# Performance work log

Hardware: AMD Instinct MI355X
Metric: run time of the kernel (lower is better)

The kernel has to match this reference:

```python
import jax, jax.numpy as jnp
import numpy as np

N_EMBD = 1024
N_HEAD = 16
STRIDE = 128
C = 8
SEQ = 2048
BATCH = 2


def _sparse_causal_mask(nd, ns, stride, c, dtype):
    # Faithful vectorization of _sparse_attention_mask:
    # column j is globally visible if (j % stride) >= stride - c (the last c
    # columns of each stride block), each query also sees its own stride block,
    # and everything is causally masked (j <= q).
    j = jnp.arange(ns)
    q = jnp.arange(ns)[:, None]
    col_sel = (j % stride) >= (stride - c)          # strided summary columns
    same_block = (j[None, :] // stride) == (q // stride)  # local block
    causal = j[None, :] <= q
    mask = ((col_sel[None, :] | same_block) & causal).astype(dtype)
    return mask[ns - nd:]


def setup_inputs() -> dict:
    key = jax.random.key(0)
    k1, k2, k3 = jax.random.split(key, 3)
    inputs = jax.random.normal(k1, (BATCH, SEQ, N_EMBD), dtype=jnp.float32)
    w_attn = jax.random.normal(k2, (N_EMBD, 3 * N_EMBD), dtype=jnp.float32) * 0.02
    b_attn = jnp.zeros((3 * N_EMBD,), dtype=jnp.float32)
    proj_std = 0.02 / np.sqrt(2 * 24)  # n_layer = 24
    w_proj = jax.random.normal(k3, (N_EMBD, N_EMBD), dtype=jnp.float32) * proj_std
    b_proj = jnp.zeros((N_EMBD,), dtype=jnp.float32)
    return {"inputs": inputs, "w_attn": w_attn, "b_attn": b_attn,
            "w_proj": w_proj, "b_proj": b_proj}


def reference(inputs, w_attn, b_attn, w_proj, b_proj):
    B, S, E = inputs.shape
    H = N_HEAD
    D = E // H
    qkv = inputs @ w_attn + b_attn                     # [B,S,3E]
    q, k, v = jnp.split(qkv, 3, axis=-1)
    def split_heads(x):
        return x.reshape(B, S, H, D).transpose(0, 2, 1, 3)  # [B,H,S,D]
    q, k, v = split_heads(q), split_heads(k), split_heads(v)
    present = jnp.stack([k, v], axis=1)                # [B,2,H,S,D]
    scale = jnp.asarray(D, q.dtype) ** 0.5
    w = jnp.einsum('bhqd,bhkd->bhqk', q, k) / scale    # [B,H,S,S]
    mask = _sparse_causal_mask(S, S, STRIDE, C, w.dtype)
    w = w * mask - 1e10 * (1.0 - mask)
    p = jax.nn.softmax(w, axis=-1).astype(v.dtype)
    h = jnp.einsum('bhqk,bhkd->bhqd', p, v)            # [B,H,S,D]
    h = h.transpose(0, 2, 1, 3).reshape(B, S, E)       # merge heads
    h = h @ w_proj + b_proj
    # dropout p=0.0 (eval) -> identity
    return (h, present)
```

## Files before the change

kernel.cpp:

```cpp
#include <hip/hip_runtime.h>
#include <stdint.h>

typedef unsigned short u16;
typedef unsigned int u32;
typedef __attribute__((ext_vector_type(4))) float f32x4;
typedef __attribute__((ext_vector_type(4))) u16 u16x4;
typedef __attribute__((ext_vector_type(8))) __bf16 bf16x8;

__device__ __forceinline__ u16 f2bf(float f) {
  u32 u = __builtin_bit_cast(u32, f);
  u = (u + 0x7FFFu + ((u >> 16) & 1u)) >> 16;
  return (u16)u;
}

__device__ __forceinline__ void gload_lds16(const void* g, void* l) {
  __builtin_amdgcn_global_load_lds(
      (const __attribute__((address_space(1))) void*)(uintptr_t)(g),
      (__attribute__((address_space(3))) void*)(u32)(uintptr_t)(l),
      16, 0, 0);
}

__global__ __launch_bounds__(256) void k_prep(
    const float* __restrict__ x, u16* __restrict__ xbf,
    const float* __restrict__ wa, u16* __restrict__ wat,
    const float* __restrict__ wp, u16* __restrict__ wpt) {
  __shared__ float tile[32][33];
  const int bid = blockIdx.x, t = threadIdx.x;
  if (bid < 4096) {
    int i = bid * 256 + t;
    f32x4 v = ((const f32x4*)x)[i];
    u16x4 o = { f2bf(v.x), f2bf(v.y), f2bf(v.z), f2bf(v.w) };
    ((u16x4*)xbf)[i] = o;
    return;
  }
  const float* in;
  u16* out;
  int n0, k0, N;
  if (bid < 4096 + 3072) {
    int idx = bid - 4096;
    in = wa; out = wat; N = 3072;
    n0 = (idx % 96) * 32; k0 = (idx / 96) * 32;
  } else {
    int idx = bid - 7168;
    in = wp; out = wpt; N = 1024;
    n0 = (idx & 31) * 32; k0 = (idx >> 5) * 32;
  }
  int c = t & 31, r0 = t >> 5;
#pragma unroll
  for (int i = 0; i < 4; ++i)
    tile[r0 + i * 8][c] = in[(size_t)(k0 + r0 + i * 8) * N + n0 + c];
  __syncthreads();
  int on = t >> 3, ok = (t & 7) * 4;
  u16x4 o = { f2bf(tile[ok + 0][on]), f2bf(tile[ok + 1][on]),
              f2bf(tile[ok + 2][on]), f2bf(tile[ok + 3][on]) };
  *(u16x4*)&out[(size_t)(n0 + on) * 1024 + k0 + ok] = o;
}

__global__ __launch_bounds__(256) void k_kv(const float* __restrict__ present,
                                            u16* __restrict__ kbf,
                                            u16* __restrict__ vtw) {
  __shared__ float tile[32][33];
  const int bid = blockIdx.x, t = threadIdx.x;
  if (bid >= 4096) {
    int i = bid - 4096;
    size_t idx = (size_t)i * 256 + t;
    size_t b = idx >> 19, off = idx & ((1u << 19) - 1);
    f32x4 v = ((const f32x4*)present)[b * (1u << 20) + off];
    u16x4 o = { f2bf(v.x), f2bf(v.y), f2bf(v.z), f2bf(v.w) };
    ((u16x4*)kbf)[idx] = o;
    return;
  }
  int bh = bid >> 7, rem = bid & 127;
  int s0 = (rem >> 1) * 32, d0 = (rem & 1) * 32;
  int b = bh >> 4, h = bh & 15;
  const float* vsrc = present + (((size_t)(b * 2 + 1) * 16 + h) * 2048) * 64;
  u16* vdst = vtw + ((size_t)bh * 64) * 2048;
  int c = t & 31, r0 = t >> 5;
#pragma unroll
  for (int i = 0; i < 4; ++i)
    tile[r0 + i * 8][c] = vsrc[(size_t)(s0 + r0 + i * 8) * 64 + d0 + c];
  __syncthreads();
  int on = t >> 3, ok = (t & 7) * 4;
  u16x4 o = { f2bf(tile[ok + 0][on]), f2bf(tile[ok + 1][on]),
              f2bf(tile[ok + 2][on]), f2bf(tile[ok + 3][on]) };
  *(u16x4*)&vdst[(size_t)(d0 + on) * 2048 + s0 + ok] = o;
}

__global__ __launch_bounds__(512, 1) void k_gemm256(
    const u16* __restrict__ A, const u16* __restrict__ Bt,
    const float* __restrict__ bias, u16* __restrict__ outq,
    float* __restrict__ outp) {
  __shared__ u16 a_lds[2][256 * 64];
  __shared__ u16 b_lds[2][192 * 64];
  const int t = threadIdx.x;
  const int lane = t & 63, w = t >> 6;
  const int cc = lane & 15, g = lane >> 4;
  const int wr = w >> 1, wc = w & 1;

  int f = blockIdx.y * 16 + blockIdx.x;
  int xcd = f & 7, idx = f >> 3;
  const int m0 = ((xcd >> 1) * 4 + (idx >> 3)) * 256;
  const int n0 = ((xcd & 1) * 8 + (idx & 7)) * 192;

  const int srow = t >> 3;
  const int scolb = (t & 7) * 16;
  const size_t pitch = 2048;

  auto stage = [&](int bi, int kt) {
#pragma unroll
    for (int i = 0; i < 3; ++i) {
      int row = i * 64 + srow;
      gload_lds16((const char*)Bt + (size_t)(n0 + row) * pitch + kt * 128 +
                      (scolb ^ ((row & 7) << 4)),
                  (char*)b_lds[bi] + row * 128 + scolb);
    }
#pragma unroll
    for (int i = 0; i < 4; ++i) {
      int row = i * 64 + srow;
      gload_lds16((const char*)A + (size_t)(m0 + row) * pitch + kt * 128 +
                      (scolb ^ ((row & 7) << 4)),
                  (char*)a_lds[bi] + row * 128 + scolb);
    }
  };

  auto readA = [&](bf16x8 (&af)[4], int bi, int kk) {
#pragma unroll
    for (int mf = 0; mf < 4; ++mf) {
      int row = wr * 64 + mf * 16 + cc;
      af[mf] = *(const bf16x8*)((const char*)a_lds[bi] + row * 128 +
                                ((kk * 64 + g * 16) ^ ((row & 7) << 4)));
    }
  };
  auto readB = [&](bf16x8 (&bf)[6], int bi, int kk) {
#pragma unroll
    for (int nf = 0; nf < 6; ++nf) {
      int row = wc * 96 + nf * 16 + cc;
      bf[nf] = *(const bf16x8*)((const char*)b_lds[bi] + row * 128 +
                                ((kk * 64 + g * 16) ^ ((row & 7) << 4)));
    }
  };

  f32x4 acc[4][6] = {};
  bf16x8 a0[4], b0[6], a1[4], b1[6];

  stage(0, 0);
  asm volatile("s_waitcnt vmcnt(0)\n\ts_barrier" ::: "memory");
  readA(a0, 0, 0);
  readB(b0, 0, 0);

  for (int j = 0; j < 16; ++j) {
    const int bi = j & 1, nx = bi ^ 1;
    if (j < 15) stage(nx, j + 1);
    readA(a1, bi, 1);
    readB(b1, bi, 1);

    __builtin_amdgcn_s_setprio(1);
#pragma unroll
    for (int mf = 0; mf < 4; ++mf)
#pragma unroll
      for (int nf = 0; nf < 6; ++nf)
        acc[mf][nf] = __builtin_amdgcn_mfma_f32_16x16x32_bf16(
            a0[mf], b0[nf], acc[mf][nf], 0, 0, 0);
    __builtin_amdgcn_s_setprio(0);

    __builtin_amdgcn_s_setprio(1);
#pragma unroll
    for (int mf = 0; mf < 4; ++mf)
#pragma unroll
      for (int nf = 0; nf < 6; ++nf)
        acc[mf][nf] = __builtin_amdgcn_mfma_f32_16x16x32_bf16(
            a1[mf], b1[nf], acc[mf][nf], 0, 0, 0);
    __builtin_amdgcn_s_setprio(0);

    if (j < 15) {
      asm volatile("s_waitcnt vmcnt(0) lgkmcnt(0)\n\ts_barrier" ::: "memory");
      readA(a0, nx, 0);
      readB(b0, nx, 0);
    }
  }

  float bv[6];
#pragma unroll
  for (int nf = 0; nf < 6; ++nf) bv[nf] = bias[n0 + wc * 96 + nf * 16 + cc];

#pragma unroll
  for (int mf = 0; mf < 4; ++mf)
#pragma unroll
    for (int nf = 0; nf < 6; ++nf) {
      int n = n0 + wc * 96 + nf * 16 + cc;
      int mb = m0 + wr * 64 + mf * 16 + g * 4;
      float v[4];
#pragma unroll
      for (int j = 0; j < 4; ++j) v[j] = acc[mf][nf][j] + bv[nf];
      if (n < 1024) {
#pragma unroll
        for (int j = 0; j < 4; ++j) outq[(size_t)(mb + j) * 1024 + n] = f2bf(v[j]);
      } else {
        int n2 = n - 1024;
        int kv = n2 >> 10; n2 &= 1023;
        int hh = n2 >> 6, d = n2 & 63;
        int bb = mb >> 11, ss = mb & 2047;
        float* pr = outp + ((((size_t)bb * 2 + kv) * 16 + hh) * 2048 + ss) * 64 + d;
#pragma unroll
        for (int j = 0; j < 4; ++j) pr[(size_t)j * 64] = v[j];
      }
    }
}

template <int EPI, int BN>
__global__ __launch_bounds__(256) void k_gemm(
    const u16* __restrict__ A, const u16* __restrict__ Bt,
    const float* __restrict__ bias, u16* __restrict__ outq,
    float* __restrict__ outp, int M, int N, int K) {
  __shared__ u16 a_lds[128 * 64];
  __shared__ u16 b_lds[BN * 64];
  const int t = threadIdx.x;
  const int lane = t & 63, w = t >> 6;

  int m0, n0;
  {
    constexpr int NXT = (EPI == 0) ? 24 : 16;
    constexpr int NCH = (EPI == 0) ? 12 : 8;
    int f = blockIdx.y * NXT + blockIdx.x;
    int xcd = f & 7, idx = f >> 3;
    int mt = (xcd >> 1) * 8 + idx / NCH;
    int nt = (xcd & 1) * NCH + idx % NCH;
    m0 = mt * 128;
    n0 = nt * BN;
  }

  const int srow = t >> 3;
  const int scb = (t & 7) * 16;
  const int ssw = scb ^ ((srow & 7) << 4);
  const size_t pitch = (size_t)K * 2;
  const char* aS = (const char*)A + (size_t)(m0 + srow) * pitch + ssw;
  const char* bS = (const char*)Bt + (size_t)(n0 + srow) * pitch + ssw;
  char* al = (char*)a_lds + t * 16;
  char* bl = (char*)b_lds + t * 16;
  const int wm = (w >> 1) * 64, wn = (w & 1) * (BN / 2);
  const int cc = lane & 15, g = lane >> 4;
  constexpr int NF = BN / 32;

  f32x4 acc[4][NF] = {};

  for (int kt = 0; kt < K; kt += 64) {
    __syncthreads();
#pragma unroll
    for (int i = 0; i < 4; ++i)
      gload_lds16(aS + (size_t)kt * 2 + (size_t)i * 32 * pitch, al + i * 4096);
#pragma unroll
    for (int i = 0; i < BN / 32; ++i)
      gload_lds16(bS + (size_t)kt * 2 + (size_t)i * 32 * pitch, bl + i * 4096);
    __syncthreads();
#pragma unroll
    for (int kk = 0; kk < 2; ++kk) {
      bf16x8 af[4], bf_[NF];
#pragma unroll
      for (int mf = 0; mf < 4; ++mf) {
        int row = wm + mf * 16 + cc;
        af[mf] = *(const bf16x8*)((const char*)a_lds + row * 128 +
                                  ((kk * 64 + g * 16) ^ ((row & 7) << 4)));
      }
#pragma unroll
      for (int nf = 0; nf < NF; ++nf) {
        int row = wn + nf * 16 + cc;
        bf_[nf] = *(const bf16x8*)((const char*)b_lds + row * 128 +
                                   ((kk * 64 + g * 16) ^ ((row & 7) << 4)));
      }
#pragma unroll
      for (int mf = 0; mf < 4; ++mf)
#pragma unroll
        for (int nf = 0; nf < NF; ++nf)
          acc[mf][nf] = __builtin_amdgcn_mfma_f32_16x16x32_bf16(
              af[mf], bf_[nf], acc[mf][nf], 0, 0, 0);
    }
  }

  float bv[NF];
#pragma unroll
  for (int nf = 0; nf < NF; ++nf) bv[nf] = bias[n0 + wn + nf * 16 + cc];

#pragma unroll
  for (int mf = 0; mf < 4; ++mf)
#pragma unroll
    for (int nf = 0; nf < NF; ++nf) {
      int n = n0 + wn + nf * 16 + cc;
      int mb = m0 + wm + mf * 16 + g * 4;
      float v[4];
#pragma unroll
      for (int j = 0; j < 4; ++j) v[j] = acc[mf][nf][j] + bv[nf];
      if (EPI == 1) {
#pragma unroll
        for (int j = 0; j < 4; ++j) outp[(size_t)(mb + j) * N + n] = v[j];
      } else if (n < 1024) {
#pragma unroll
        for (int j = 0; j < 4; ++j) outq[(size_t)(mb + j) * 1024 + n] = f2bf(v[j]);
      } else {
        int n2 = n - 1024;
        int kv = n2 >> 10; n2 &= 1023;
        int hh = n2 >> 6, d = n2 & 63;
        int bb = mb >> 11, ss = mb & 2047;
        float* pr = outp + ((((size_t)bb * 2 + kv) * 16 + hh) * 2048 + ss) * 64 + d;
#pragma unroll
        for (int j = 0; j < 4; ++j) pr[(size_t)j * 64] = v[j];
      }
    }
}

__global__ __launch_bounds__(256) void k_attn(
    const u16* __restrict__ qws, const u16* __restrict__ kbf,
    const u16* __restrict__ vtw, u16* __restrict__ hws) {
  const int qb = blockIdx.x, h = blockIdx.y, b = blockIdx.z;
  const int t = threadIdx.x, lane = t & 63, w = t >> 6;
  const int cc = lane & 15, g = lane >> 4;

  __shared__ u16 k_lds[256 * 64];
  __shared__ u16 p_lds[4][32 * 72];
  __shared__ float rsum[4][32];

  const char* kh = (const char*)kbf + (size_t)(b * 16 + h) * (2048 * 128);
  const char* vh = (const char*)vtw + (size_t)(b * 16 + h) * (64 * 4096);

  {
    int rr = t >> 3, seg = (t & 7) * 16;
#pragma unroll
    for (int i = 0; i < 8; ++i) {
      int r = i * 32 + rr;
      int i2 = r - 128;
      int gr = (r < 128) ? (qb * 128 + r) : ((i2 >> 3) * 128 + 120 + (i2 & 7));
      gload_lds16(kh + (size_t)gr * 128 + (seg ^ ((r & 7) << 4)),
                  (char*)k_lds + i * 4096 + t * 16);
    }
  }

  bf16x8 qf_[2][2];
  {
    const char* qsrc = (const char*)qws +
        (size_t)(b * 2048 + qb * 128 + w * 32 + cc) * 2048 + h * 128 + g * 16;
#pragma unroll
    for (int qf = 0; qf < 2; ++qf)
#pragma unroll
      for (int kk = 0; kk < 2; ++kk)
        qf_[qf][kk] = *(const bf16x8*)(qsrc + (size_t)qf * 16 * 2048 + kk * 64);
  }
  __syncthreads();

  const int nsum = 8 * qb;
  f32x4 o_[2][4] = {};
  float lsum[2] = { 0.f, 0.f };

#pragma unroll 2
  for (int ch = 0; ch < 4; ++ch) {
    f32x4 s[4][2] = {};
#pragma unroll
    for (int kf2 = 0; kf2 < 4; ++kf2) {
      int row = ch * 64 + kf2 * 16 + cc;
      const char* kr = (const char*)k_lds + row * 128;
#pragma unroll
      for (int kk = 0; kk < 2; ++kk) {
        bf16x8 kfr = *(const bf16x8*)(kr + ((kk * 64 + g * 16) ^ ((cc & 7) << 4)));
#pragma unroll
        for (int qf = 0; qf < 2; ++qf)
          s[kf2][qf] = __builtin_amdgcn_mfma_f32_16x16x32_bf16(
              kfr, qf_[qf][kk], s[kf2][qf], 0, 0, 0);
      }
    }
#pragma unroll
    for (int qf = 0; qf < 2; ++qf) {
      int q_local = w * 32 + qf * 16 + cc;
#pragma unroll
      for (int kf2 = 0; kf2 < 4; ++kf2) {
#pragma unroll
        for (int j = 0; j < 4; ++j) {
          int key = ch * 64 + kf2 * 16 + g * 4 + j;
          bool vis = (key < 128) ? (key <= q_local) : (key - 128 < nsum);
          float p = vis ? exp2f(s[kf2][qf][j] * 0.180336884f) : 0.f;
          s[kf2][qf][j] = p;
          lsum[qf] += p;
        }
        u16x4 pw = { f2bf(s[kf2][qf][0]), f2bf(s[kf2][qf][1]),
                     f2bf(s[kf2][qf][2]), f2bf(s[kf2][qf][3]) };
        *(u16x4*)&p_lds[w][(qf * 16 + cc) * 72 + kf2 * 16 + g * 4] = pw;
      }
    }
#pragma unroll
    for (int kk = 0; kk < 2; ++kk) {
      bf16x8 pa[2], vb[4];
#pragma unroll
      for (int mf = 0; mf < 2; ++mf)
        pa[mf] = *(const bf16x8*)((const char*)p_lds[w] +
                                  (mf * 16 + cc) * 144 + kk * 64 + g * 16);
      int cb = (ch < 2) ? (qb * 256 + ch * 128 + kk * 64 + g * 16)
                        : (((ch - 2) * 8 + kk * 4 + g) * 256 + 240);
#pragma unroll
      for (int nf = 0; nf < 4; ++nf)
        vb[nf] = *(const bf16x8*)(vh + (size_t)(nf * 16 + cc) * 4096 + cb);
#pragma unroll
      for (int mf = 0; mf < 2; ++mf)
#pragma unroll
        for (int nf = 0; nf < 4; ++nf)
          o_[mf][nf] = __builtin_amdgcn_mfma_f32_16x16x32_bf16(pa[mf], vb[nf],
                                                               o_[mf][nf], 0, 0, 0);
    }
  }

#pragma unroll
  for (int qf = 0; qf < 2; ++qf) {
    float sum = lsum[qf];
    sum += __shfl_xor(sum, 16);
    sum += __shfl_xor(sum, 32);
    if (g == 0) rsum[w][qf * 16 + cc] = sum;
  }
#pragma unroll
  for (int mf = 0; mf < 2; ++mf)
#pragma unroll
    for (int j = 0; j < 4; ++j) {
      float inv = 1.0f / rsum[w][mf * 16 + g * 4 + j];
      size_t row = (size_t)(b * 2048 + qb * 128 + w * 32 + mf * 16 + g * 4 + j);
#pragma unroll
      for (int nf = 0; nf < 4; ++nf)
        hws[row * 1024 + h * 64 + nf * 16 + cc] = f2bf(o_[mf][nf][j] * inv);
    }
}

extern "C" void kernel_launch(void* const* d_in, const int* in_sizes, int n_in,
                              void* d_out, int out_size, void* d_ws, size_t ws_size,
                              hipStream_t stream) {
  const float* x      = (const float*)d_in[0];
  const float* w_attn = (const float*)d_in[1];
  const float* b_attn = (const float*)d_in[2];
  const float* w_proj = (const float*)d_in[3];
  const float* b_proj = (const float*)d_in[4];
  float* h_out   = (float*)d_out;
  float* present = (float*)d_out + 4194304;

  char* ws = (char*)d_ws;
  u16* xbf = (u16*)(ws);
  u16* qws = (u16*)(ws + (8u << 20));
  u16* wat = (u16*)(ws + (16u << 20));
  u16* wpt = (u16*)(ws + (22u << 20));
  u16* kbf = (u16*)(ws + (24u << 20));
  u16* vtw = (u16*)(ws + (32u << 20));
  u16* hws = xbf;

  k_prep<<<8192, 256, 0, stream>>>(x, xbf, w_attn, wat, w_proj, wpt);
  k_gemm256<<<dim3(16, 16), 512, 0, stream>>>(xbf, wat, b_attn, qws, present);
  k_kv<<<8192, 256, 0, stream>>>(present, kbf, vtw);
  k_attn<<<dim3(16, 16, 2), 256, 0, stream>>>(qws, kbf, vtw, hws);
  k_gemm<1, 64><<<dim3(16, 32), 256, 0, stream>>>(hws, wpt, b_proj, nullptr,
                                                  h_out, 4096, 1024, 1024);
}
```

Before: 86.50 us.

## Replace double-buffered GEMM K-loop with single-buffered 128-wide K tiles

```diff
diff --git a/kernel.cpp b/kernel.cpp
--- a/kernel.cpp
+++ b/kernel.cpp
@@ -90,8 +90,8 @@
     const u16* __restrict__ A, const u16* __restrict__ Bt,
     const float* __restrict__ bias, u16* __restrict__ outq,
     float* __restrict__ outp) {
-  __shared__ u16 a_lds[2][256 * 64];
-  __shared__ u16 b_lds[2][192 * 64];
+  __shared__ u16 a_lds[256 * 128];
+  __shared__ u16 b_lds[192 * 128];
   const int t = threadIdx.x;
   const int lane = t & 63, w = t >> 6;
   const int cc = lane & 15, g = lane >> 4;
@@ -102,80 +102,54 @@
   const int m0 = ((xcd >> 1) * 4 + (idx >> 3)) * 256;
   const int n0 = ((xcd & 1) * 8 + (idx & 7)) * 192;
 
-  const int srow = t >> 3;
-  const int scolb = (t & 7) * 16;
+  const int srow = t >> 4;
+  const int scolb = (t & 15) * 16;
   const size_t pitch = 2048;
 
-  auto stage = [&](int bi, int kt) {
-#pragma unroll
-    for (int i = 0; i < 3; ++i) {
-      int row = i * 64 + srow;
-      gload_lds16((const char*)Bt + (size_t)(n0 + row) * pitch + kt * 128 +
+  auto stage = [&](int kt) {
+#pragma unroll
+    for (int i = 0; i < 8; ++i) {
+      int row = i * 32 + srow;
+      gload_lds16((const char*)A + (size_t)(m0 + row) * pitch + kt * 256 +
                       (scolb ^ ((row & 7) << 4)),
-                  (char*)b_lds[bi] + row * 128 + scolb);
-    }
-#pragma unroll
-    for (int i = 0; i < 4; ++i) {
-      int row = i * 64 + srow;
-      gload_lds16((const char*)A + (size_t)(m0 + row) * pitch + kt * 128 +
+                  (char*)a_lds + row * 256 + scolb);
+    }
+#pragma unroll
+    for (int i = 0; i < 6; ++i) {
+      int row = i * 32 + srow;
+      gload_lds16((const char*)Bt + (size_t)(n0 + row) * pitch + kt * 256 +
                       (scolb ^ ((row & 7) << 4)),
-                  (char*)a_lds[bi] + row * 128 + scolb);
+                  (char*)b_lds + row * 256 + scolb);
     }
   };
 
-  auto readA = [&](bf16x8 (&af)[4], int bi, int kk) {
-#pragma unroll
-    for (int mf = 0; mf < 4; ++mf) {
-      int row = wr * 64 + mf * 16 + cc;
-      af[mf] = *(const bf16x8*)((const char*)a_lds[bi] + row * 128 +
-                                ((kk * 64 + g * 16) ^ ((row & 7) << 4)));
-    }
-  };
-  auto readB = [&](bf16x8 (&bf)[6], int bi, int kk) {
-#pragma unroll
-    for (int nf = 0; nf < 6; ++nf) {
-      int row = wc * 96 + nf * 16 + cc;
-      bf[nf] = *(const bf16x8*)((const char*)b_lds[bi] + row * 128 +
-                                ((kk * 64 + g * 16) ^ ((row & 7) << 4)));
-    }
-  };
-
   f32x4 acc[4][6] = {};
-  bf16x8 a0[4], b0[6], a1[4], b1[6];
-
-  stage(0, 0);
-  asm volatile("s_waitcnt vmcnt(0)\n\ts_barrier" ::: "memory");
-  readA(a0, 0, 0);
-  readB(b0, 0, 0);
-
-  for (int j = 0; j < 16; ++j) {
-    const int bi = j & 1, nx = bi ^ 1;
-    if (j < 15) stage(nx, j + 1);
-    readA(a1, bi, 1);
-    readB(b1, bi, 1);
-
-    __builtin_amdgcn_s_setprio(1);
-#pragma unroll
-    for (int mf = 0; mf < 4; ++mf)
-#pragma unroll
-      for (int nf = 0; nf < 6; ++nf)
-        acc[mf][nf] = __builtin_amdgcn_mfma_f32_16x16x32_bf16(
-            a0[mf], b0[nf], acc[mf][nf], 0, 0, 0);
-    __builtin_amdgcn_s_setprio(0);
-
-    __builtin_amdgcn_s_setprio(1);
-#pragma unroll
-    for (int mf = 0; mf < 4; ++mf)
-#pragma unroll
-      for (int nf = 0; nf < 6; ++nf)
-        acc[mf][nf] = __builtin_amdgcn_mfma_f32_16x16x32_bf16(
-            a1[mf], b1[nf], acc[mf][nf], 0, 0, 0);
-    __builtin_amdgcn_s_setprio(0);
-
-    if (j < 15) {
-      asm volatile("s_waitcnt vmcnt(0) lgkmcnt(0)\n\ts_barrier" ::: "memory");
-      readA(a0, nx, 0);
-      readB(b0, nx, 0);
+
+  for (int kt = 0; kt < 8; ++kt) {
+    __syncthreads();
+    stage(kt);
+    __syncthreads();
+#pragma unroll
+    for (int kk = 0; kk < 4; ++kk) {
+      bf16x8 af[4], bf_[6];
+#pragma unroll
+      for (int mf = 0; mf < 4; ++mf) {
+        int row = wr * 64 + mf * 16 + cc;
+        af[mf] = *(const bf16x8*)((const char*)a_lds + row * 256 +
+                                  ((kk * 64 + g * 16) ^ ((row & 7) << 4)));
+      }
+#pragma unroll
+      for (int nf = 0; nf < 6; ++nf) {
+        int row = wc * 96 + nf * 16 + cc;
+        bf_[nf] = *(const bf16x8*)((const char*)b_lds + row * 256 +
+                                   ((kk * 64 + g * 16) ^ ((row & 7) << 4)));
+      }
+#pragma unroll
+      for (int mf = 0; mf < 4; ++mf)
+#pragma unroll
+        for (int nf = 0; nf < 6; ++nf)
+          acc[mf][nf] = __builtin_amdgcn_mfma_f32_16x16x32_bf16(
+              af[mf], bf_[nf], acc[mf][nf], 0, 0, 0);
     }
   }
 
```

New measurement: 92.28 us. +6.7%, slower.

## Load GEMM B operand directly from global into registers, bypassing LDS

Applied to the files above, without the earlier changes.

```diff
diff --git a/kernel.cpp b/kernel.cpp
--- a/kernel.cpp
+++ b/kernel.cpp
@@ -91,7 +91,6 @@
     const float* __restrict__ bias, u16* __restrict__ outq,
     float* __restrict__ outp) {
   __shared__ u16 a_lds[2][256 * 64];
-  __shared__ u16 b_lds[2][192 * 64];
   const int t = threadIdx.x;
   const int lane = t & 63, w = t >> 6;
   const int cc = lane & 15, g = lane >> 4;
@@ -106,14 +105,7 @@
   const int scolb = (t & 7) * 16;
   const size_t pitch = 2048;
 
-  auto stage = [&](int bi, int kt) {
-#pragma unroll
-    for (int i = 0; i < 3; ++i) {
-      int row = i * 64 + srow;
-      gload_lds16((const char*)Bt + (size_t)(n0 + row) * pitch + kt * 128 +
-                      (scolb ^ ((row & 7) << 4)),
-                  (char*)b_lds[bi] + row * 128 + scolb);
-    }
+  auto stageA = [&](int bi, int kt) {
 #pragma unroll
     for (int i = 0; i < 4; ++i) {
       int row = i * 64 + srow;
@@ -122,7 +114,16 @@
                   (char*)a_lds[bi] + row * 128 + scolb);
     }
   };
-
+  const char* bbase = (const char*)Bt +
+      (size_t)(n0 + wc * 96 + cc) * pitch + g * 16;
+  auto loadB = [&](bf16x8 (&bf)[6][2], int kt) {
+#pragma unroll
+    for (int nf = 0; nf < 6; ++nf)
+#pragma unroll
+      for (int kk = 0; kk < 2; ++kk)
+        bf[nf][kk] = *(const bf16x8*)(bbase + (size_t)(nf * 16) * pitch +
+                                      kt * 128 + kk * 64);
+  };
   auto readA = [&](bf16x8 (&af)[4], int bi, int kk) {
 #pragma unroll
     for (int mf = 0; mf < 4; ++mf) {
@@ -131,51 +132,59 @@
                                 ((kk * 64 + g * 16) ^ ((row & 7) << 4)));
     }
   };
-  auto readB = [&](bf16x8 (&bf)[6], int bi, int kk) {
-#pragma unroll
-    for (int nf = 0; nf < 6; ++nf) {
-      int row = wc * 96 + nf * 16 + cc;
-      bf[nf] = *(const bf16x8*)((const char*)b_lds[bi] + row * 128 +
-                                ((kk * 64 + g * 16) ^ ((row & 7) << 4)));
-    }
-  };
 
   f32x4 acc[4][6] = {};
-  bf16x8 a0[4], b0[6], a1[4], b1[6];
-
-  stage(0, 0);
-  asm volatile("s_waitcnt vmcnt(0)\n\ts_barrier" ::: "memory");
+  bf16x8 a0[4], a1[4];
+  bf16x8 bX[6][2], bY[6][2];
+
+  stageA(0, 0);
+  loadB(bX, 0);
+  asm volatile("s_waitcnt vmcnt(12)\n\ts_barrier" ::: "memory");
   readA(a0, 0, 0);
-  readB(b0, 0, 0);
-
-  for (int j = 0; j < 16; ++j) {
-    const int bi = j & 1, nx = bi ^ 1;
-    if (j < 15) stage(nx, j + 1);
-    readA(a1, bi, 1);
-    readB(b1, bi, 1);
-
+  readA(a1, 0, 1);
+
+#pragma unroll 1
+  for (int jj = 0; jj < 8; ++jj) {
+    const int j0 = jj * 2, j1 = j0 + 1;
+    if (j0 < 15) { stageA(1, j0 + 1); loadB(bY, j0 + 1); }
     __builtin_amdgcn_s_setprio(1);
 #pragma unroll
     for (int mf = 0; mf < 4; ++mf)
 #pragma unroll
       for (int nf = 0; nf < 6; ++nf)
         acc[mf][nf] = __builtin_amdgcn_mfma_f32_16x16x32_bf16(
-            a0[mf], b0[nf], acc[mf][nf], 0, 0, 0);
-    __builtin_amdgcn_s_setprio(0);
-
-    __builtin_amdgcn_s_setprio(1);
+            a0[mf], bX[nf][0], acc[mf][nf], 0, 0, 0);
 #pragma unroll
     for (int mf = 0; mf < 4; ++mf)
 #pragma unroll
       for (int nf = 0; nf < 6; ++nf)
         acc[mf][nf] = __builtin_amdgcn_mfma_f32_16x16x32_bf16(
-            a1[mf], b1[nf], acc[mf][nf], 0, 0, 0);
+            a1[mf], bX[nf][1], acc[mf][nf], 0, 0, 0);
     __builtin_amdgcn_s_setprio(0);
-
-    if (j < 15) {
-      asm volatile("s_waitcnt vmcnt(0) lgkmcnt(0)\n\ts_barrier" ::: "memory");
-      readA(a0, nx, 0);
-      readB(b0, nx, 0);
+    if (j0 < 15) {
+      asm volatile("s_waitcnt vmcnt(12)\n\ts_barrier" ::: "memory");
+      readA(a0, 1, 0);
+      readA(a1, 1, 1);
+    }
+    if (j1 < 15) { stageA(0, j1 + 1); loadB(bX, j1 + 1); }
+    __builtin_amdgcn_s_setprio(1);
+#pragma unroll
+    for (int mf = 0; mf < 4; ++mf)
+#pragma unroll
+      for (int nf = 0; nf < 6; ++nf)
+        acc[mf][nf] = __builtin_amdgcn_mfma_f32_16x16x32_bf16(
+            a0[mf], bY[nf][0], acc[mf][nf], 0, 0, 0);
+#pragma unroll
+    for (int mf = 0; mf < 4; ++mf)
+#pragma unroll
+      for (int nf = 0; nf < 6; ++nf)
+        acc[mf][nf] = __builtin_amdgcn_mfma_f32_16x16x32_bf16(
+            a1[mf], bY[nf][1], acc[mf][nf], 0, 0, 0);
+    __builtin_amdgcn_s_setprio(0);
+    if (j1 < 15) {
+      asm volatile("s_waitcnt vmcnt(12)\n\ts_barrier" ::: "memory");
+      readA(a0, 0, 0);
+      readA(a1, 0, 1);
     }
   }
 
```

New measurement: 145.3 us. +68.0%, slower.
